# Optimization experiments

Measured on AMD Instinct MI355X. Metric: run time of the kernel, lower is better.

Reference implementation:

```python
import jax, jax.numpy as jnp
import numpy as np

M = 8192      # nodes
D = 128       # feature dim
DEG = 32      # neighbors per node


def setup_inputs() -> dict:
    key = jax.random.key(0)
    ks = jax.random.split(key, 6)
    z = jax.random.normal(ks[0], (M, D), dtype=jnp.float32)
    # deterministic, duplicate-free edge list: node i -> (i+1..i+DEG) mod M
    src = jnp.repeat(jnp.arange(M, dtype=jnp.int64), DEG)
    dst = (src + jnp.tile(jnp.arange(1, DEG + 1, dtype=jnp.int64), M)) % M
    edge_index = jnp.stack([src, dst], axis=0)  # [2, M*DEG]
    s = 1.0 / np.sqrt(D)
    Wg = jax.random.normal(ks[1], (D, D), dtype=jnp.float32) * s
    Wc = jax.random.normal(ks[2], (D, D), dtype=jnp.float32) * s
    Wq = jax.random.normal(ks[3], (D, D), dtype=jnp.float32) * s
    Wk = jax.random.normal(ks[4], (D, D), dtype=jnp.float32) * s
    a = jax.random.normal(ks[5], (2 * D,), dtype=jnp.float32)
    return {"z": z, "edge_index": edge_index, "Wg": Wg, "Wc": Wc,
            "Wq": Wq, "Wk": Wk, "a": a}


def reference(z, edge_index, Wg, Wc, Wq, Wk, a):
    m, d = z.shape
    wg = z @ Wg.T                              # [m, d]
    src, dst = edge_index[0], edge_index[1]
    a_src, a_dst = a[:d], a[d:]
    # per-edge score: leaky_relu(a . [wg[i], wg[j]]) = leaky_relu(a1.wg[i] + a2.wg[j])
    scores = jax.nn.leaky_relu((wg @ a_src)[src] + (wg @ a_dst)[dst])  # [E]
    # softmax over each source node's neighbors (segment softmax)
    smax = jax.ops.segment_max(scores, src, num_segments=m)
    ex = jnp.exp(scores - smax[src])
    denom = jax.ops.segment_sum(ex, src, num_segments=m)
    alpha = ex / denom[src]                    # [E]
    # scatter-aggregate: local[i] = sum_j alpha_ij * wg[j]
    local = jax.ops.segment_sum(alpha[:, None] * wg[dst], src, num_segments=m)
    # dense global attention branch
    q = z @ Wq.T
    k = z @ Wk.T
    beta = jax.nn.softmax(q @ k.T / jnp.sqrt(jnp.float32(d)), axis=-1)  # [m, m]
    global_msg = beta @ (z @ Wc.T)
    return jax.nn.leaky_relu(local + global_msg + z)
```

## Files before the change

kernel.cpp:

```cpp
#include <hip/hip_runtime.h>

#define MM 8192
#define DD 128
#define DEG 32
#define KSPLIT 8
#define NB 16
#define RSTAGE 48

typedef __attribute__((ext_vector_type(8))) _Float16 h8;
typedef __attribute__((ext_vector_type(4))) float f4;
typedef __attribute__((ext_vector_type(4))) unsigned int u4;
typedef __attribute__((ext_vector_type(4))) short s4;

__device__ __forceinline__ unsigned short f2h(float f) {
  _Float16 h = (_Float16)f;
  return __builtin_bit_cast(unsigned short, h);
}

__device__ __forceinline__ void lds_dma16(const unsigned short* gptr, unsigned short* lptr) {
  __builtin_amdgcn_global_load_lds(
      (const __attribute__((address_space(1))) unsigned int*)gptr,
      (__attribute__((address_space(3))) unsigned int*)lptr, 16, 0, 0);
}

__global__ __launch_bounds__(256) void proj_kernel(
    const float* __restrict__ z, const float* __restrict__ Wg,
    const float* __restrict__ Wc, const float* __restrict__ Wq,
    const float* __restrict__ Wk, const float* __restrict__ a,
    float* __restrict__ wg, unsigned short* __restrict__ qb,
    unsigned short* __restrict__ kb, unsigned short* __restrict__ ct,
    float* __restrict__ sg, float* __restrict__ sd)
{
  __shared__ unsigned short zt[64 * 136];
  __shared__ unsigned short wt[128 * 136];
  const int mode = blockIdx.y;
  const float* __restrict__ W = (mode == 0) ? Wg : (mode == 1) ? Wq : (mode == 2) ? Wk : Wc;
  const int r0 = blockIdx.x * 64;
  const int tid = threadIdx.x;

  #pragma unroll
  for (int it = 0; it < 8; ++it) {
    int id = tid + it * 256, row = id >> 5, c4 = (id & 31) * 4;
    f4 v = *(const f4*)(z + (r0 + row) * DD + c4);
    s4 sv = {(short)f2h(v.x), (short)f2h(v.y), (short)f2h(v.z), (short)f2h(v.w)};
    *(s4*)&zt[row * 136 + c4] = sv;
  }
  #pragma unroll
  for (int it = 0; it < 16; ++it) {
    int id = tid + it * 256, row = id >> 5, c4 = (id & 31) * 4;
    f4 v = *(const f4*)(W + row * DD + c4);
    s4 sv = {(short)f2h(v.x), (short)f2h(v.y), (short)f2h(v.z), (short)f2h(v.w)};
    *(s4*)&wt[row * 136 + c4] = sv;
  }
  __syncthreads();

  const int lane = tid & 63, w = tid >> 6, n = lane & 15, quad = lane >> 4;
  h8 afr[4];
  #pragma unroll
  for (int kt = 0; kt < 4; ++kt)
    afr[kt] = *(const h8*)&zt[(16 * w + n) * 136 + kt * 32 + quad * 8];

  f4 acc[8];
  const f4 fzero = {0.f, 0.f, 0.f, 0.f};
  #pragma unroll
  for (int nt = 0; nt < 8; ++nt) {
    f4 c = fzero;
    #pragma unroll
    for (int kt = 0; kt < 4; ++kt) {
      h8 b = *(const h8*)&wt[(16 * nt + n) * 136 + kt * 32 + quad * 8];
      c = __builtin_amdgcn_mfma_f32_16x16x32_f16(afr[kt], b, c, 0, 0, 0);
    }
    acc[nt] = c;
  }

  if (mode == 0) {
    #pragma unroll
    for (int nt = 0; nt < 8; ++nt)
      #pragma unroll
      for (int r = 0; r < 4; ++r)
        wg[(r0 + 16 * w + quad * 4 + r) * DD + 16 * nt + n] = acc[nt][r];
    float av[8], bv[8];
    #pragma unroll
    for (int nt = 0; nt < 8; ++nt) { av[nt] = a[16 * nt + n]; bv[nt] = a[DD + 16 * nt + n]; }
    #pragma unroll
    for (int r = 0; r < 4; ++r) {
      float s1 = 0.f, s2 = 0.f;
      #pragma unroll
      for (int nt = 0; nt < 8; ++nt) { s1 += acc[nt][r] * av[nt]; s2 += acc[nt][r] * bv[nt]; }
      s1 += __shfl_xor(s1, 1); s1 += __shfl_xor(s1, 2); s1 += __shfl_xor(s1, 4); s1 += __shfl_xor(s1, 8);
      s2 += __shfl_xor(s2, 1); s2 += __shfl_xor(s2, 2); s2 += __shfl_xor(s2, 4); s2 += __shfl_xor(s2, 8);
      if (n == 0) {
        int g = r0 + 16 * w + quad * 4 + r;
        sg[g] = s1; sd[g] = s2;
      }
    }
  } else if (mode == 1) {
    const float qscale = 0.08838834764831845f;
    #pragma unroll
    for (int nt = 0; nt < 8; ++nt)
      #pragma unroll
      for (int r = 0; r < 4; ++r)
        qb[(r0 + 16 * w + quad * 4 + r) * DD + 16 * nt + n] = f2h(acc[nt][r] * qscale);
  } else if (mode == 2) {
    #pragma unroll
    for (int nt = 0; nt < 8; ++nt)
      #pragma unroll
      for (int r = 0; r < 4; ++r)
        kb[(r0 + 16 * w + quad * 4 + r) * DD + 16 * nt + n] = f2h(acc[nt][r]);
  } else {
    __syncthreads();
    #pragma unroll
    for (int nt = 0; nt < 8; ++nt)
      #pragma unroll
      for (int r = 0; r < 4; ++r)
        wt[(16 * nt + n) * 80 + 16 * w + quad * 4 + r] = f2h(acc[nt][r]);
    __syncthreads();
    #pragma unroll
    for (int it = 0; it < 4; ++it) {
      int idx = tid + it * 256, d = idx >> 3, c8 = (idx & 7) * 8;
      u4 v = *(const u4*)&wt[d * 80 + c8];
      *(u4*)(ct + (size_t)d * MM + r0 + c8) = v;
    }
  }
}

__global__ __launch_bounds__(256, 2) void flash_kernel(
    const unsigned short* __restrict__ qb, const unsigned short* __restrict__ kb,
    const unsigned short* __restrict__ ct, unsigned short* __restrict__ Opart,
    float* __restrict__ Lpart)
{
  __shared__ unsigned short sh[37376];
  const int bx = blockIdx.x, ck = blockIdx.y;
  const int tid = threadIdx.x, lane = tid & 63, w = tid >> 6;
  const int n = lane & 15, quad = lane >> 4;
  const int ln = n, lq = quad;
  const int qr0 = bx * 128;

  #pragma unroll
  for (int it = 0; it < 8; ++it)
    lds_dma16(qb + (qr0 + it * 16 + ln) * DD + w * 32 + lq * 8,
              &sh[(it * 256 + tid) * 8]);
  __syncthreads();
  h8 aq[2][4];
  #pragma unroll
  for (int mt = 0; mt < 2; ++mt)
    #pragma unroll
    for (int kt = 0; kt < 4; ++kt)
      aq[mt][kt] = *(const h8*)&sh[((w * 2 + mt) * 4 + kt) * 512 + lane * 8];
  __syncthreads();

  const unsigned short* kp = kb + (size_t)(ck * 1024 + 4 * ln) * DD + w * 32 + lq * 8;
  const unsigned short* vp = ct + (size_t)(16 * (w >> 1) + ln) * MM + ck * 1024 + (w & 1) * 32 + lq * 8;

  #pragma unroll
  for (int it = 0; it < 4; ++it)
    lds_dma16(kp + it * DD, &sh[(it * 256 + tid) * 8]);
  #pragma unroll
  for (int it = 0; it < 4; ++it)
    lds_dma16(vp + (size_t)it * 32 * MM, &sh[8192 + (it * 256 + tid) * 8]);

  f4 acc_o[2][8];
  const f4 fzero = {0.f, 0.f, 0.f, 0.f};
  #pragma unroll
  for (int mt = 0; mt < 2; ++mt)
    #pragma unroll
    for (int dt = 0; dt < 8; ++dt) acc_o[mt][dt] = fzero;
  float l_r[2][4] = {{0.f, 0.f, 0.f, 0.f}, {0.f, 0.f, 0.f, 0.f}};
  const int pbase = 32768 + w * 1152;

  for (int t = 0; t < 16; ++t) {
    __syncthreads();
    const int cur = (t & 1) * 16384;

    if (t < 15) {
      const int nb = ((t + 1) & 1) * 16384;
      const unsigned short* kpn = kp + (size_t)(t + 1) * 64 * DD;
      const unsigned short* vpn = vp + (t + 1) * 64;
      #pragma unroll
      for (int it = 0; it < 4; ++it)
        lds_dma16(kpn + it * DD, &sh[nb + (it * 256 + tid) * 8]);
      #pragma unroll
      for (int it = 0; it < 4; ++it)
        lds_dma16(vpn + (size_t)it * 32 * MM, &sh[nb + 8192 + (it * 256 + tid) * 8]);
    }

    f4 accs[2][4];
    #pragma unroll
    for (int mt = 0; mt < 2; ++mt)
      #pragma unroll
      for (int nt = 0; nt < 4; ++nt) accs[mt][nt] = fzero;
    #pragma unroll
    for (int nt = 0; nt < 4; ++nt) {
      #pragma unroll
      for (int kt = 0; kt < 4; ++kt) {
        h8 bk = *(const h8*)&sh[cur + nt * 2048 + kt * 512 + lane * 8];
        accs[0][nt] = __builtin_amdgcn_mfma_f32_16x16x32_f16(aq[0][kt], bk, accs[0][nt], 0, 0, 0);
        accs[1][nt] = __builtin_amdgcn_mfma_f32_16x16x32_f16(aq[1][kt], bk, accs[1][nt], 0, 0, 0);
      }
    }

    h8 ap[2][2];
    #pragma unroll
    for (int mt = 0; mt < 2; ++mt) {
      #pragma unroll
      for (int r = 0; r < 4; ++r) {
        float p0 = __expf(fminf(accs[mt][0][r], 10.f));
        float p1 = __expf(fminf(accs[mt][1][r], 10.f));
        float p2 = __expf(fminf(accs[mt][2][r], 10.f));
        float p3 = __expf(fminf(accs[mt][3][r], 10.f));
        l_r[mt][r] += p0 + p1 + p2 + p3;
        unsigned int lo = ((unsigned int)f2h(p1) << 16) | f2h(p0);
        unsigned int hi = ((unsigned int)f2h(p3) << 16) | f2h(p2);
        uint2 pv; pv.x = lo; pv.y = hi;
        *(uint2*)&sh[pbase + (quad * 4 + r) * 72 + n * 4] = pv;
      }
      ap[mt][0] = *(const h8*)&sh[pbase + n * 72 + quad * 8];
      ap[mt][1] = *(const h8*)&sh[pbase + n * 72 + 32 + quad * 8];
    }

    #pragma unroll
    for (int dt = 0; dt < 8; ++dt) {
      #pragma unroll
      for (int k2 = 0; k2 < 2; ++k2) {
        h8 bv = *(const h8*)&sh[cur + 8192 + dt * 1024 + k2 * 512 + lane * 8];
        acc_o[0][dt] = __builtin_amdgcn_mfma_f32_16x16x32_f16(ap[0][k2], bv, acc_o[0][dt], 0, 0, 0);
        acc_o[1][dt] = __builtin_amdgcn_mfma_f32_16x16x32_f16(ap[1][k2], bv, acc_o[1][dt], 0, 0, 0);
      }
    }
  }

  #pragma unroll
  for (int mt = 0; mt < 2; ++mt)
    #pragma unroll
    for (int r = 0; r < 4; ++r) {
      float lv = l_r[mt][r];
      lv += __shfl_xor(lv, 1); lv += __shfl_xor(lv, 2);
      lv += __shfl_xor(lv, 4); lv += __shfl_xor(lv, 8);
      int g = qr0 + w * 32 + mt * 16 + quad * 4 + r;
      if (n == 0) Lpart[ck * MM + g] = lv;
      #pragma unroll
      for (int dt = 0; dt < 8; ++dt)
        Opart[((size_t)ck * MM + g) * DD + 16 * dt + n] = f2h(acc_o[mt][dt][r]);
    }
}

__global__ __launch_bounds__(256) void merge_kernel(
    const int* __restrict__ ei, const float* __restrict__ wg,
    const float* __restrict__ sg, const float* __restrict__ sd,
    const unsigned short* __restrict__ Opart, const float* __restrict__ Lpart,
    const float* __restrict__ z, float* __restrict__ out)
{
  __shared__ float rows_s[RSTAGE * 132];
  __shared__ float sc_s[NB][DEG];
  __shared__ float alpha_s[NB][DEG];
  __shared__ int idx_s[NB][DEG];
  const int tid = threadIdx.x;
  const int i0 = blockIdx.x * NB;

  #pragma unroll
  for (int it = 0; it < 6; ++it) {
    int idx = tid + it * 256;
    int r = idx >> 5, c4 = (idx & 31) * 4;
    int grow = (i0 + 1 + r) & (MM - 1);
    *(f4*)&rows_s[r * 132 + c4] = *(const f4*)(wg + (size_t)grow * DD + c4);
  }
  #pragma unroll
  for (int it = 0; it < 2; ++it) {
    int e = tid + it * 256;
    int ni = e >> 5, j = e & 31;
    int i = i0 + ni;
    int dstj = ei[MM * DEG + i * DEG + j];
    float s = sg[i] + sd[dstj];
    sc_s[ni][j] = s > 0.f ? s : 0.01f * s;
    idx_s[ni][j] = (dstj - (i0 + 1)) & (MM - 1);
  }
  __syncthreads();

  if (tid < NB) {
    float mx = -1e30f;
    #pragma unroll 8
    for (int j = 0; j < DEG; ++j) mx = fmaxf(mx, sc_s[tid][j]);
    float sum = 0.f;
    #pragma unroll 8
    for (int j = 0; j < DEG; ++j) { float p = __expf(sc_s[tid][j] - mx); alpha_s[tid][j] = p; sum += p; }
    float inv = 1.f / sum;
    #pragma unroll 8
    for (int j = 0; j < DEG; ++j) alpha_s[tid][j] *= inv;
  }
  __syncthreads();

  const int ni = tid >> 4, d0 = (tid & 15) * 8;
  const int i = i0 + ni;
  float acc[8] = {0.f, 0.f, 0.f, 0.f, 0.f, 0.f, 0.f, 0.f};
  #pragma unroll 4
  for (int j = 0; j < DEG; ++j) {
    float al = alpha_s[ni][j];
    int r = idx_s[ni][j];
    if (r < RSTAGE) {
      const float* src = &rows_s[r * 132 + d0];
      #pragma unroll
      for (int q = 0; q < 8; ++q) acc[q] += al * src[q];
    } else {
      const float* src = wg + (size_t)((i0 + 1 + r) & (MM - 1)) * DD + d0;
      #pragma unroll
      for (int q = 0; q < 8; ++q) acc[q] += al * src[q];
    }
  }

  float l = 0.f;
  float o[8] = {0.f, 0.f, 0.f, 0.f, 0.f, 0.f, 0.f, 0.f};
  #pragma unroll
  for (int ck = 0; ck < KSPLIT; ++ck) {
    l += Lpart[ck * MM + i];
    h8 v = *(const h8*)(Opart + ((size_t)ck * MM + i) * DD + d0);
    #pragma unroll
    for (int q = 0; q < 8; ++q) o[q] += (float)v[q];
  }
  float inv = 1.0f / l;
  const float* zp = z + (size_t)i * DD + d0;
  float* op = out + (size_t)i * DD + d0;
  #pragma unroll
  for (int q = 0; q < 8; ++q) {
    float r = o[q] * inv + acc[q] + zp[q];
    op[q] = r > 0.f ? r : 0.01f * r;
  }
}

extern "C" void kernel_launch(void* const* d_in, const int* in_sizes, int n_in,
                              void* d_out, int out_size, void* d_ws, size_t ws_size,
                              hipStream_t stream) {
  const float* z  = (const float*)d_in[0];
  const int*   ei = (const int*)d_in[1];
  const float* Wg = (const float*)d_in[2];
  const float* Wc = (const float*)d_in[3];
  const float* Wq = (const float*)d_in[4];
  const float* Wk = (const float*)d_in[5];
  const float* a  = (const float*)d_in[6];
  float* out = (float*)d_out;
  char* ws = (char*)d_ws;

  float*          wg    = (float*)(ws + 0);
  unsigned short* qb    = (unsigned short*)(ws + (4 << 20));
  unsigned short* kb    = (unsigned short*)(ws + (6 << 20));
  unsigned short* ct    = (unsigned short*)(ws + (8 << 20));
  float*          sg    = (float*)(ws + (10 << 20));
  float*          sd    = (float*)(ws + (10 << 20) + (64 << 10));
  unsigned short* Opart = (unsigned short*)(ws + (15 << 20));
  float*          Lpart = (float*)(ws + (31 << 20));

  proj_kernel<<<dim3(128, 4), 256, 0, stream>>>(z, Wg, Wc, Wq, Wk, a, wg, qb, kb, ct, sg, sd);
  flash_kernel<<<dim3(64, KSPLIT), 256, 0, stream>>>(qb, kb, ct, Opart, Lpart);
  merge_kernel<<<512, 256, 0, stream>>>(ei, wg, sg, sd, Opart, Lpart, z, out);
}
```

Measured before the change: 126.7 us.

## Shrink flash tiles to 32 keys, double KSPLIT, raise occupancy, use exp2

```diff
diff --git a/kernel.cpp b/kernel.cpp
--- a/kernel.cpp
+++ b/kernel.cpp
@@ -3,7 +3,9 @@
 #define MM 8192
 #define DD 128
 #define DEG 32
-#define KSPLIT 8
+#define KSPLIT 16
+#define BK 32
+#define NTILE 16
 #define NB 16
 #define RSTAGE 48
 
@@ -95,7 +97,7 @@
       }
     }
   } else if (mode == 1) {
-    const float qscale = 0.08838834764831845f;
+    const float qscale = 0.12752551286084110f;
     #pragma unroll
     for (int nt = 0; nt < 8; ++nt)
       #pragma unroll
@@ -124,17 +126,18 @@
   }
 }
 
-__global__ __launch_bounds__(256, 2) void flash_kernel(
+__global__ __launch_bounds__(256, 4) void flash_kernel(
     const unsigned short* __restrict__ qb, const unsigned short* __restrict__ kb,
     const unsigned short* __restrict__ ct, unsigned short* __restrict__ Opart,
     float* __restrict__ Lpart)
 {
-  __shared__ unsigned short sh[37376];
-  const int bx = blockIdx.x, ck = blockIdx.y;
+  __shared__ unsigned short sh[18944];
+  const int bid = blockIdx.x + (blockIdx.y << 6);
+  const int ck = bid & 15, qt = bid >> 4;
   const int tid = threadIdx.x, lane = tid & 63, w = tid >> 6;
   const int n = lane & 15, quad = lane >> 4;
   const int ln = n, lq = quad;
-  const int qr0 = bx * 128;
+  const int qr0 = qt * 128;
 
   #pragma unroll
   for (int it = 0; it < 8; ++it)
@@ -149,15 +152,15 @@
       aq[mt][kt] = *(const h8*)&sh[((w * 2 + mt) * 4 + kt) * 512 + lane * 8];
   __syncthreads();
 
-  const unsigned short* kp = kb + (size_t)(ck * 1024 + 4 * ln) * DD + w * 32 + lq * 8;
-  const unsigned short* vp = ct + (size_t)(16 * (w >> 1) + ln) * MM + ck * 1024 + (w & 1) * 32 + lq * 8;
-
-  #pragma unroll
-  for (int it = 0; it < 4; ++it)
+  const unsigned short* kp = kb + (size_t)(ck * 512 + 2 * ln) * DD + w * 32 + lq * 8;
+  const unsigned short* vp = ct + (size_t)(16 * w + ln) * MM + ck * 512 + lq * 8;
+
+  #pragma unroll
+  for (int it = 0; it < 2; ++it)
     lds_dma16(kp + it * DD, &sh[(it * 256 + tid) * 8]);
   #pragma unroll
-  for (int it = 0; it < 4; ++it)
-    lds_dma16(vp + (size_t)it * 32 * MM, &sh[8192 + (it * 256 + tid) * 8]);
+  for (int it = 0; it < 2; ++it)
+    lds_dma16(vp + (size_t)it * 64 * MM, &sh[4096 + (it * 256 + tid) * 8]);
 
   f4 acc_o[2][8];
   const f4 fzero = {0.f, 0.f, 0.f, 0.f};
@@ -166,31 +169,29 @@
     #pragma unroll
     for (int dt = 0; dt < 8; ++dt) acc_o[mt][dt] = fzero;
   float l_r[2][4] = {{0.f, 0.f, 0.f, 0.f}, {0.f, 0.f, 0.f, 0.f}};
-  const int pbase = 32768 + w * 1152;
-
-  for (int t = 0; t < 16; ++t) {
+  const int pbase = 16384 + w * 640;
+
+  for (int t = 0; t < NTILE; ++t) {
     __syncthreads();
-    const int cur = (t & 1) * 16384;
-
-    if (t < 15) {
-      const int nb = ((t + 1) & 1) * 16384;
-      const unsigned short* kpn = kp + (size_t)(t + 1) * 64 * DD;
-      const unsigned short* vpn = vp + (t + 1) * 64;
-      #pragma unroll
-      for (int it = 0; it < 4; ++it)
+    const int cur = (t & 1) * 8192;
+
+    if (t < NTILE - 1) {
+      const int nb = ((t + 1) & 1) * 8192;
+      const unsigned short* kpn = kp + (size_t)(t + 1) * BK * DD;
+      const unsigned short* vpn = vp + (t + 1) * BK;
+      #pragma unroll
+      for (int it = 0; it < 2; ++it)
         lds_dma16(kpn + it * DD, &sh[nb + (it * 256 + tid) * 8]);
       #pragma unroll
-      for (int it = 0; it < 4; ++it)
-        lds_dma16(vpn + (size_t)it * 32 * MM, &sh[nb + 8192 + (it * 256 + tid) * 8]);
-    }
-
-    f4 accs[2][4];
-    #pragma unroll
-    for (int mt = 0; mt < 2; ++mt)
-      #pragma unroll
-      for (int nt = 0; nt < 4; ++nt) accs[mt][nt] = fzero;
-    #pragma unroll
-    for (int nt = 0; nt < 4; ++nt) {
+      for (int it = 0; it < 2; ++it)
+        lds_dma16(vpn + (size_t)it * 64 * MM, &sh[nb + 4096 + (it * 256 + tid) * 8]);
+    }
+
+    f4 accs[2][2];
+    accs[0][0] = fzero; accs[0][1] = fzero; accs[1][0] = fzero; accs[1][1] = fzero;
+    __builtin_amdgcn_s_setprio(1);
+    #pragma unroll
+    for (int nt = 0; nt < 2; ++nt) {
       #pragma unroll
       for (int kt = 0; kt < 4; ++kt) {
         h8 bk = *(const h8*)&sh[cur + nt * 2048 + kt * 512 + lane * 8];
@@ -198,35 +199,31 @@
         accs[1][nt] = __builtin_amdgcn_mfma_f32_16x16x32_f16(aq[1][kt], bk, accs[1][nt], 0, 0, 0);
       }
     }
-
-    h8 ap[2][2];
+    __builtin_amdgcn_s_setprio(0);
+
+    h8 ap[2];
     #pragma unroll
     for (int mt = 0; mt < 2; ++mt) {
       #pragma unroll
       for (int r = 0; r < 4; ++r) {
-        float p0 = __expf(fminf(accs[mt][0][r], 10.f));
-        float p1 = __expf(fminf(accs[mt][1][r], 10.f));
-        float p2 = __expf(fminf(accs[mt][2][r], 10.f));
-        float p3 = __expf(fminf(accs[mt][3][r], 10.f));
-        l_r[mt][r] += p0 + p1 + p2 + p3;
-        unsigned int lo = ((unsigned int)f2h(p1) << 16) | f2h(p0);
-        unsigned int hi = ((unsigned int)f2h(p3) << 16) | f2h(p2);
-        uint2 pv; pv.x = lo; pv.y = hi;
-        *(uint2*)&sh[pbase + (quad * 4 + r) * 72 + n * 4] = pv;
+        float p0 = exp2f(fminf(accs[mt][0][r], 14.4269504f));
+        float p1 = exp2f(fminf(accs[mt][1][r], 14.4269504f));
+        l_r[mt][r] += p0 + p1;
+        auto pv = __builtin_amdgcn_cvt_pkrtz(p0, p1);
+        *(unsigned int*)&sh[pbase + (quad * 4 + r) * 40 + 2 * n] =
+            __builtin_bit_cast(unsigned int, pv);
       }
-      ap[mt][0] = *(const h8*)&sh[pbase + n * 72 + quad * 8];
-      ap[mt][1] = *(const h8*)&sh[pbase + n * 72 + 32 + quad * 8];
-    }
-
+      ap[mt] = *(const h8*)&sh[pbase + n * 40 + quad * 8];
+    }
+
+    __builtin_amdgcn_s_setprio(1);
     #pragma unroll
     for (int dt = 0; dt < 8; ++dt) {
-      #pragma unroll
-      for (int k2 = 0; k2 < 2; ++k2) {
-        h8 bv = *(const h8*)&sh[cur + 8192 + dt * 1024 + k2 * 512 + lane * 8];
-        acc_o[0][dt] = __builtin_amdgcn_mfma_f32_16x16x32_f16(ap[0][k2], bv, acc_o[0][dt], 0, 0, 0);
-        acc_o[1][dt] = __builtin_amdgcn_mfma_f32_16x16x32_f16(ap[1][k2], bv, acc_o[1][dt], 0, 0, 0);
-      }
-    }
+      h8 bv = *(const h8*)&sh[cur + 4096 + dt * 512 + lane * 8];
+      acc_o[0][dt] = __builtin_amdgcn_mfma_f32_16x16x32_f16(ap[0], bv, acc_o[0][dt], 0, 0, 0);
+      acc_o[1][dt] = __builtin_amdgcn_mfma_f32_16x16x32_f16(ap[1], bv, acc_o[1][dt], 0, 0, 0);
+    }
+    __builtin_amdgcn_s_setprio(0);
   }
 
   #pragma unroll
@@ -267,29 +264,31 @@
   #pragma unroll
   for (int it = 0; it < 2; ++it) {
     int e = tid + it * 256;
-    int ni = e >> 5, j = e & 31;
-    int i = i0 + ni;
+    int nj = e >> 5, j = e & 31;
+    int i = i0 + nj;
     int dstj = ei[MM * DEG + i * DEG + j];
     float s = sg[i] + sd[dstj];
-    sc_s[ni][j] = s > 0.f ? s : 0.01f * s;
-    idx_s[ni][j] = (dstj - (i0 + 1)) & (MM - 1);
+    sc_s[nj][j] = s > 0.f ? s : 0.01f * s;
+    idx_s[nj][j] = (dstj - (i0 + 1)) & (MM - 1);
   }
   __syncthreads();
 
-  if (tid < NB) {
-    float mx = -1e30f;
-    #pragma unroll 8
-    for (int j = 0; j < DEG; ++j) mx = fmaxf(mx, sc_s[tid][j]);
-    float sum = 0.f;
-    #pragma unroll 8
-    for (int j = 0; j < DEG; ++j) { float p = __expf(sc_s[tid][j] - mx); alpha_s[tid][j] = p; sum += p; }
+  const int ni = tid >> 4, l16 = tid & 15;
+  {
+    float s0 = sc_s[ni][l16], s1 = sc_s[ni][l16 + 16];
+    float mx = fmaxf(s0, s1);
+    mx = fmaxf(mx, __shfl_xor(mx, 1)); mx = fmaxf(mx, __shfl_xor(mx, 2));
+    mx = fmaxf(mx, __shfl_xor(mx, 4)); mx = fmaxf(mx, __shfl_xor(mx, 8));
+    float p0 = __expf(s0 - mx), p1 = __expf(s1 - mx);
+    float sum = p0 + p1;
+    sum += __shfl_xor(sum, 1); sum += __shfl_xor(sum, 2);
+    sum += __shfl_xor(sum, 4); sum += __shfl_xor(sum, 8);
     float inv = 1.f / sum;
-    #pragma unroll 8
-    for (int j = 0; j < DEG; ++j) alpha_s[tid][j] *= inv;
-  }
-  __syncthreads();
-
-  const int ni = tid >> 4, d0 = (tid & 15) * 8;
+    alpha_s[ni][l16] = p0 * inv;
+    alpha_s[ni][l16 + 16] = p1 * inv;
+  }
+
+  const int d0 = l16 * 8;
   const int i = i0 + ni;
   float acc[8] = {0.f, 0.f, 0.f, 0.f, 0.f, 0.f, 0.f, 0.f};
   #pragma unroll 4
@@ -345,8 +344,8 @@
   unsigned short* ct    = (unsigned short*)(ws + (8 << 20));
   float*          sg    = (float*)(ws + (10 << 20));
   float*          sd    = (float*)(ws + (10 << 20) + (64 << 10));
-  unsigned short* Opart = (unsigned short*)(ws + (15 << 20));
-  float*          Lpart = (float*)(ws + (31 << 20));
+  unsigned short* Opart = (unsigned short*)(ws + (11 << 20));
+  float*          Lpart = (float*)(ws + (43 << 20));
 
   proj_kernel<<<dim3(128, 4), 256, 0, stream>>>(z, Wg, Wc, Wq, Wk, a, wg, qb, kb, ct, sg, sd);
   flash_kernel<<<dim3(64, KSPLIT), 256, 0, stream>>>(qb, kb, ct, Opart, Lpart);
```

New measurement: 174.1 us. 37.4% more time.
